# Performance work log

Hardware: AMD Instinct MI355X
Metric: run time of the kernel (lower is better)

The kernel has to match this reference:

```python
import jax, jax.numpy as jnp
import numpy as np

H = 768; B = 8; T = 1024; V = 50257
S = 256      # token_distribution_samples
K = 64       # token_topk
POOL = 1024  # max(S*4, K) token pool
TEMP = 0.1; LIM = 0.25; MW = 0.1


def _ln(x, g, b):
    m = x.mean(-1, keepdims=True)
    v = ((x - m) ** 2).mean(-1, keepdims=True)
    return (x - m) / jnp.sqrt(v + 1e-5) * g + b


def _head(x, g, b, w1, b1, w2, b2):
    # LayerNorm -> Linear -> GELU(exact) -> (Dropout=identity in eval) -> Linear
    h = _ln(x, g, b) @ w1 + b1
    h = jax.nn.gelu(h, approximate=False)
    return h @ w2 + b2


def _l2norm(x):
    return x / jnp.maximum(jnp.linalg.norm(x, axis=-1, keepdims=True), 1e-12)


def setup_inputs() -> dict:
    key = jax.random.key(0)
    ks = jax.random.split(key, 16)
    init = lambda k, shp: jax.random.normal(k, shp, jnp.float32) * 0.02
    f32 = jnp.float32
    return {
        "latent": jax.random.normal(ks[0], (B, T, H), f32),
        "token_embedding_matrix": jax.random.normal(ks[1], (V, H), f32),
        # scale head
        "scale_ln_g": jnp.ones((H,), f32), "scale_ln_b": jnp.zeros((H,), f32),
        "scale_w1": init(ks[2], (H, H)), "scale_b1": jnp.zeros((H,), f32),
        "scale_w2": init(ks[3], (H, H)), "scale_b2": jnp.zeros((H,), f32),
        # bias head
        "bias_ln_g": jnp.ones((H,), f32), "bias_ln_b": jnp.zeros((H,), f32),
        "bias_w1": init(ks[4], (H, H)), "bias_b1": jnp.zeros((H,), f32),
        "bias_w2": init(ks[5], (H, H)), "bias_b2": jnp.zeros((H,), f32),
        # contrastive head (projection_dim == H)
        "con_ln_g": jnp.ones((H,), f32), "con_ln_b": jnp.zeros((H,), f32),
        "con_w1": init(ks[6], (H, H)), "con_b1": jnp.zeros((H,), f32),
        "con_w2": init(ks[7], (H, H)), "con_b2": jnp.zeros((H,), f32),
        # deterministic augmentation noise (randn_like * 0.01)
        "noise_a": jax.random.normal(ks[8], (B * T, H), f32) * 0.01,
        "noise_b": jax.random.normal(ks[9], (B * T, H), f32) * 0.01,
        # deterministic row-sampling (torch.randperm analogues)
        "samp_idx": jax.random.permutation(ks[10], B * T)[:S].astype(jnp.int32),
        "tok_idx": jax.random.permutation(ks[11], V)[:POOL].astype(jnp.int32),
    }


def reference(latent, token_embedding_matrix,
              scale_ln_g, scale_ln_b, scale_w1, scale_b1, scale_w2, scale_b2,
              bias_ln_g, bias_ln_b, bias_w1, bias_b1, bias_w2, bias_b2,
              con_ln_g, con_ln_b, con_w1, con_b1, con_w2, con_b2,
              noise_a, noise_b, samp_idx, tok_idx):
    # compensate: u = s(z)*z + b(z)
    scale = 1.0 + LIM * jnp.tanh(_head(latent, scale_ln_g, scale_ln_b, scale_w1, scale_b1, scale_w2, scale_b2))
    bias = LIM * jnp.tanh(_head(latent, bias_ln_g, bias_ln_b, bias_w1, bias_b1, bias_w2, bias_b2))
    aligned = scale * latent + bias

    flat = aligned.reshape(-1, H)  # [N, H], N = B*T
    # contrastive loss
    va = _l2norm(_head(flat + noise_a, con_ln_g, con_ln_b, con_w1, con_b1, con_w2, con_b2))
    vb = _l2norm(_head(flat + noise_b, con_ln_g, con_ln_b, con_w1, con_b1, con_w2, con_b2))
    logits = va @ vb.T / TEMP  # [N, N]
    loss_ab = -jnp.mean(jnp.diagonal(jax.nn.log_softmax(logits, axis=-1)))
    loss_ba = -jnp.mean(jnp.diagonal(jax.nn.log_softmax(logits.T, axis=-1)))
    con_loss = 0.5 * (loss_ab + loss_ba)

    # token distribution loss
    af = flat[samp_idx]                     # [S, H]
    te = token_embedding_matrix[tok_idx]    # [POOL, H]
    tl = _l2norm(af) @ _l2norm(te).T / TEMP  # [S, POOL]
    top_vals, top_idx = jax.lax.top_k(tl, K)
    top_emb = te[top_idx]                   # [S, K, H] gather
    w = jax.nn.softmax(top_vals, axis=-1)[..., None]
    proto = (w * top_emb).sum(axis=1)       # [S, H]
    proto_loss = jnp.mean((af - proto) ** 2)
    moment_loss = jnp.mean((af.mean(0) - te.mean(0)) ** 2) \
        + jnp.mean((af.std(0) - te.std(0)) ** 2)
    token_dist_loss = proto_loss + MW * moment_loss

    comp_reg_loss = jnp.mean((scale - 1.0) ** 2) + jnp.mean(bias ** 2)
    return (aligned, con_loss, token_dist_loss, comp_reg_loss, scale, bias)
```

## Files before the change

### kernel.cpp

```cpp
#include <hip/hip_runtime.h>
#include <hip/hip_bf16.h>

typedef __hip_bfloat16 bf16;
typedef __attribute__((ext_vector_type(4))) float f32x4;
typedef __attribute__((ext_vector_type(8))) short bf16x8v;

static constexpr int   HD    = 768;
static constexpr int   NRr   = 8192;
static constexpr int   SSAMP = 256;
static constexpr int   KTOP  = 64;
static constexpr int   NPOOL = 1024;
static constexpr float TINV  = 10.0f;

__device__ __forceinline__ float bf2f(bf16 h){ return __bfloat162float(h); }
__device__ __forceinline__ bf16  f2bf(float f){ return __float2bfloat16(f); }

__device__ __forceinline__ float gelu_exact(float x){
  return 0.5f * x * (1.0f + erff(x * 0.70710678118654752f));
}

__device__ __forceinline__ float block_sum(float v, float* buf){
  const int lane = threadIdx.x & 63, w = threadIdx.x >> 6;
  const int nw = (int)blockDim.x >> 6;
  #pragma unroll
  for(int o = 32; o; o >>= 1) v += __shfl_down(v, o);
  __syncthreads();
  if(lane == 0) buf[w] = v;
  __syncthreads();
  float t = 0.f;
  for(int i = 0; i < nw; i++) t += buf[i];
  return t;
}

__device__ __forceinline__ void block_sum2(float& a, float& b, float* buf){
  const int lane = threadIdx.x & 63, w = threadIdx.x >> 6;
  #pragma unroll
  for(int o = 32; o; o >>= 1){ a += __shfl_down(a, o); b += __shfl_down(b, o); }
  __syncthreads();
  if(lane == 0){ buf[w] = a; buf[4 + w] = b; }
  __syncthreads();
  float ta = 0.f, tb = 0.f;
  #pragma unroll
  for(int i = 0; i < 4; i++){ ta += buf[i]; tb += buf[4 + i]; }
  a = ta; b = tb;
}

__device__ __forceinline__ void gload_lds16(const bf16* g, bf16* lds_uniform){
  __builtin_amdgcn_global_load_lds(
      (const __attribute__((address_space(1))) unsigned int*)(const void*)g,
      (__attribute__((address_space(3))) unsigned int*)(void*)lds_uniform,
      16, 0, 0);
}

struct TsA { const float* w[6]; const float* gg[6]; bf16* o[6]; };
__global__ __launch_bounds__(256)
void tscale6(TsA a){
  __shared__ float t[32][33];
  const int z = blockIdx.z;
  const float* Win = a.w[z];
  const float* g   = a.gg[z];
  bf16* Wt         = a.o[z];
  const int tx = threadIdx.x, ty = threadIdx.y;
  const int bx = blockIdx.x * 32, by = blockIdx.y * 32;
  #pragma unroll
  for(int j = 0; j < 4; j++)
    t[ty + j*8][tx] = Win[(size_t)(by + ty + j*8) * HD + bx + tx];
  __syncthreads();
  const float gv = g ? g[by + tx] : 1.0f;
  #pragma unroll
  for(int j = 0; j < 4; j++)
    Wt[(size_t)(bx + ty + j*8) * HD + by + tx] = f2bf(gv * t[tx][ty + j*8]);
}

struct FbA { const float* bln[3]; const float* w1[3]; const float* b1[3]; float* o[3]; };
__global__ __launch_bounds__(256)
void foldbias3(FbA a){
  __shared__ float red[4][64];
  const int h = blockIdx.y;
  const int lane = threadIdx.x & 63, w = threadIdx.x >> 6;
  const int n = blockIdx.x * 64 + lane;
  const float* bl = a.bln[h];
  const float* w1 = a.w1[h];
  float t = 0.f;
  for(int k = w * 192; k < w * 192 + 192; k++)
    t += bl[k] * w1[(size_t)k * HD + n];
  red[w][lane] = t;
  __syncthreads();
  if(w == 0)
    a.o[h][n] = a.b1[h][n] + red[0][lane] + red[1][lane] + red[2][lane] + red[3][lane];
}

__global__ __launch_bounds__(256)
void lnxh_kernel(const float* __restrict__ x, bf16* __restrict__ o){
  __shared__ float buf[4];
  const int row = blockIdx.x, tid = threadIdx.x;
  const size_t base = (size_t)row * HD;
  float v[3];
  #pragma unroll
  for(int j = 0; j < 3; j++) v[j] = x[base + tid + j*256];
  float s = v[0] + v[1] + v[2];
  s = block_sum(s, buf);
  const float m = s * (1.0f / HD);
  float q = 0.f;
  #pragma unroll
  for(int j = 0; j < 3; j++){ const float d = v[j] - m; q += d*d; }
  q = block_sum(q, buf);
  const float inv = rsqrtf(q * (1.0f / HD) + 1e-5f);
  #pragma unroll
  for(int j = 0; j < 3; j++)
    o[base + tid + j*256] = f2bf((v[j] - m) * inv);
}

__global__ __launch_bounds__(256)
void fuse_al_ln(const float* __restrict__ latent, const float* __restrict__ sc,
                const float* __restrict__ bi, const float* __restrict__ na,
                const float* __restrict__ nb, float* __restrict__ out_aligned,
                bf16* __restrict__ X){
  __shared__ float buf[8];
  const int row = blockIdx.x, tid = threadIdx.x;
  const size_t base = (size_t)row * HD;
  float ua[3], ub[3];
  #pragma unroll
  for(int j = 0; j < 3; j++){
    const int i = tid + j*256;
    const float a = sc[base + i] * latent[base + i] + bi[base + i];
    out_aligned[base + i] = a;
    ua[j] = a + na[base + i];
    ub[j] = a + nb[base + i];
  }
  float sa = ua[0] + ua[1] + ua[2];
  float sb = ub[0] + ub[1] + ub[2];
  block_sum2(sa, sb, buf);
  const float ma = sa * (1.0f / HD), mb = sb * (1.0f / HD);
  float qa = 0.f, qb = 0.f;
  #pragma unroll
  for(int j = 0; j < 3; j++){
    const float da = ua[j] - ma; qa += da*da;
    const float db = ub[j] - mb; qb += db*db;
  }
  block_sum2(qa, qb, buf);
  const float ia = rsqrtf(qa * (1.0f / HD) + 1e-5f);
  const float ib = rsqrtf(qb * (1.0f / HD) + 1e-5f);
  #pragma unroll
  for(int j = 0; j < 3; j++){
    const int i = tid + j*256;
    X[base + i] = f2bf((ua[j] - ma) * ia);
    X[(size_t)(row + NRr) * HD + i] = f2bf((ub[j] - mb) * ib);
  }
}

enum { EPI_GELU = 0, EPI_SB = 1, EPI_RAW = 3, EPI_LOGITS = 4, EPI_TL = 5 };

template<int EPI>
__global__ __launch_bounds__(256, 2)
void gemm_kernel(const bf16* __restrict__ A, const bf16* __restrict__ Bt,
                 const bf16* __restrict__ Bt2,
                 const int M, const int N, const int K,
                 const int lda, const int ldc,
                 const float* __restrict__ bias, const float* __restrict__ bias2,
                 bf16* __restrict__ outb, float* __restrict__ outf,
                 float* __restrict__ outf2,
                 float* __restrict__ aux, float* __restrict__ aux2){
  __shared__ __align__(16) bf16 As[128 * 64];
  __shared__ __align__(16) bf16 Bs[128 * 64];
  __shared__ float rbuf[512];

  const int tid  = threadIdx.x;
  const int wave = tid >> 6, lane = tid & 63;
  const int wm = wave >> 1, wn = wave & 1;
  const int r16 = lane & 15, kh = lane >> 4;
  const int bx = blockIdx.x, by = blockIdx.y;
  const int row0 = by * 128, col0 = bx * 128;

  float addv = 0.f;
  if constexpr(EPI == EPI_SB){
    if(blockIdx.z == 0){ addv = 1.0f; }
    else { A += 768; Bt = Bt2; bias = bias2; outf = outf2; }
  }

  f32x4 acc[4][4];
  #pragma unroll
  for(int i = 0; i < 4; i++)
    #pragma unroll
    for(int j = 0; j < 4; j++){ f32x4 z = {0.f,0.f,0.f,0.f}; acc[i][j] = z; }

  const bf16* gA[4]; const bf16* gB[4];
  bf16* lA[4]; bf16* lB[4];
  #pragma unroll
  for(int j = 0; j < 4; j++){
    const int c = tid + j*256;
    const int rr = c >> 3, p = c & 7;
    const int g = (p - (rr & 7)) & 7;
    gA[j] = A  + (size_t)(row0 + rr) * lda + g * 8;
    gB[j] = Bt + (size_t)(col0 + rr) * K   + g * 8;
    lA[j] = As + ((size_t)j*256 + wave*64) * 8;
    lB[j] = Bs + ((size_t)j*256 + wave*64) * 8;
  }
  const int sw = r16 & 7;

  for(int k0 = 0; k0 < K; k0 += 64){
    __syncthreads();
    #pragma unroll
    for(int j = 0; j < 4; j++){
      gload_lds16(gA[j] + k0, lA[j]);
      gload_lds16(gB[j] + k0, lB[j]);
    }
    __syncthreads();
    #pragma unroll
    for(int kk = 0; kk < 2; kk++){
      const int koff = ((kk*4 + kh + sw) & 7) * 8;
      bf16x8v av[4], bv[4];
      #pragma unroll
      for(int f = 0; f < 4; f++){
        av[f] = *(const bf16x8v*)(As + (wm*64 + f*16 + r16) * 64 + koff);
        bv[f] = *(const bf16x8v*)(Bs + (wn*64 + f*16 + r16) * 64 + koff);
      }
      #pragma unroll
      for(int i = 0; i < 4; i++)
        #pragma unroll
        for(int j = 0; j < 4; j++)
          acc[i][j] = __builtin_amdgcn_mfma_f32_16x16x32_bf16(av[i], bv[j], acc[i][j], 0, 0, 0);
    }
  }

  const int crow0 = row0 + wm * 64;
  const int ccol0 = col0 + wn * 64;

  if constexpr(EPI != EPI_LOGITS){
    float part = 0.f;
    #pragma unroll
    for(int i = 0; i < 4; i++){
      #pragma unroll
      for(int j = 0; j < 4; j++){
        const int col = ccol0 + j*16 + r16;
        const float bvv = bias ? bias[col] : 0.f;
        #pragma unroll
        for(int q = 0; q < 4; q++){
          const int row = crow0 + i*16 + kh*4 + q;
          const float v = acc[i][j][q] + bvv;
          const size_t off = (size_t)row * ldc + col;
          if constexpr(EPI == EPI_GELU){
            outb[off] = f2bf(gelu_exact(v));
          } else if constexpr(EPI == EPI_SB){
            const float t = 0.25f * tanhf(v);
            outf[off] = t + addv;
            part += t * t;
          } else if constexpr(EPI == EPI_TL){
            outf[off] = v * TINV;
          } else {
            outb[off] = f2bf(v);
          }
        }
      }
    }
    if constexpr(EPI == EPI_SB){
      const float tot2 = block_sum(part, rbuf);
      if(tid == 0)
        aux[(size_t)blockIdx.z * (gridDim.x * gridDim.y) + by * gridDim.x + bx] = tot2;
    }
  } else {
    float rs[16], cs[4];
    #pragma unroll
    for(int t = 0; t < 16; t++) rs[t] = 0.f;
    #pragma unroll
    for(int t = 0; t < 4; t++) cs[t] = 0.f;
    #pragma unroll
    for(int i = 0; i < 4; i++)
      #pragma unroll
      for(int j = 0; j < 4; j++)
        #pragma unroll
        for(int q = 0; q < 4; q++){
          const float ev = expf(acc[i][j][q] * TINV);
          rs[i*4 + q] += ev;
          cs[j]       += ev;
        }
    #pragma unroll
    for(int t = 0; t < 16; t++){
      float r = rs[t];
      r += __shfl_xor(r, 1); r += __shfl_xor(r, 2);
      r += __shfl_xor(r, 4); r += __shfl_xor(r, 8);
      rs[t] = r;
    }
    if(r16 == 0){
      #pragma unroll
      for(int i = 0; i < 4; i++)
        #pragma unroll
        for(int q = 0; q < 4; q++)
          rbuf[wn*128 + wm*64 + i*16 + kh*4 + q] = rs[i*4 + q];
    }
    #pragma unroll
    for(int j = 0; j < 4; j++){
      float c = cs[j];
      c += __shfl_xor(c, 16); c += __shfl_xor(c, 32);
      cs[j] = c;
    }
    if(kh == 0){
      #pragma unroll
      for(int j = 0; j < 4; j++)
        rbuf[256 + wm*128 + wn*64 + j*16 + r16] = cs[j];
    }
    __syncthreads();
    if(tid < 128){
      aux [(size_t)bx * M + row0 + tid] = rbuf[tid]       + rbuf[128 + tid];
      aux2[(size_t)by * M + col0 + tid] = rbuf[256 + tid] + rbuf[384 + tid];
    }
  }
}

__global__ __launch_bounds__(256)
void l2n_kernel(bf16* __restrict__ vio){
  __shared__ float buf[4];
  const int row = blockIdx.x, tid = threadIdx.x;
  const size_t base = (size_t)row * HD;
  float v[3];
  #pragma unroll
  for(int j = 0; j < 3; j++) v[j] = bf2f(vio[base + tid + j*256]);
  float q = v[0]*v[0] + v[1]*v[1] + v[2]*v[2];
  q = block_sum(q, buf);
  const float inv = 1.0f / fmaxf(sqrtf(q), 1e-12f);
  #pragma unroll
  for(int j = 0; j < 3; j++) vio[base + tid + j*256] = f2bf(v[j] * inv);
}

__global__ __launch_bounds__(256)
void rcdiag_kernel(const float* __restrict__ rp, const float* __restrict__ cp,
                   float* __restrict__ rs, float* __restrict__ cs, const int nb,
                   const bf16* __restrict__ va, const bf16* __restrict__ vb,
                   float* __restrict__ diag){
  if(blockIdx.x < 32){
    const int i = blockIdx.x * 256 + threadIdx.x;
    float r = 0.f, c = 0.f;
    for(int b = 0; b < nb; b++){
      r += rp[(size_t)b * NRr + i];
      c += cp[(size_t)b * NRr + i];
    }
    rs[i] = r; cs[i] = c;
  } else {
    const int lane = threadIdx.x & 63;
    const int row = (blockIdx.x - 32) * 4 + (threadIdx.x >> 6);
    const size_t base = (size_t)row * HD;
    float d = 0.f;
    #pragma unroll
    for(int j = 0; j < 12; j++){
      const int i = lane + j*64;
      d += bf2f(va[base + i]) * bf2f(vb[base + i]);
    }
    #pragma unroll
    for(int o = 32; o; o >>= 1) d += __shfl_down(d, o);
    if(lane == 0) diag[row] = d * TINV;
  }
}

__global__ __launch_bounds__(256)
void gather_kernel(const float* __restrict__ aligned, const int* __restrict__ samp,
                   float* __restrict__ afraw, bf16* __restrict__ afn,
                   const float* __restrict__ emb, const int* __restrict__ tok,
                   float* __restrict__ teg, bf16* __restrict__ ten){
  __shared__ float buf[4];
  const int tid = threadIdx.x;
  if(blockIdx.x < SSAMP){
    const int s = blockIdx.x;
    const size_t src = (size_t)samp[s] * HD, dst = (size_t)s * HD;
    float v[3];
    #pragma unroll
    for(int j = 0; j < 3; j++){
      const int i = tid + j*256;
      v[j] = aligned[src + i];
      afraw[dst + i] = v[j];
    }
    float q = v[0]*v[0] + v[1]*v[1] + v[2]*v[2];
    q = block_sum(q, buf);
    const float inv = 1.0f / fmaxf(sqrtf(q), 1e-12f);
    #pragma unroll
    for(int j = 0; j < 3; j++) afn[dst + tid + j*256] = f2bf(v[j] * inv);
  } else {
    const int p = blockIdx.x - SSAMP;
    const size_t src = (size_t)tok[p] * HD, dst = (size_t)p * HD;
    float v[3];
    #pragma unroll
    for(int j = 0; j < 3; j++){
      const int i = tid + j*256;
      v[j] = emb[src + i];
      teg[dst + i] = v[j];
    }
    float q = v[0]*v[0] + v[1]*v[1] + v[2]*v[2];
    q = block_sum(q, buf);
    const float inv = 1.0f / fmaxf(sqrtf(q), 1e-12f);
    #pragma unroll
    for(int j = 0; j < 3; j++) ten[dst + tid + j*256] = f2bf(v[j] * inv);
  }
}

__global__ __launch_bounds__(256)
void topk_kernel(const float* __restrict__ tl, const float* __restrict__ teg,
                 const float* __restrict__ afraw, float* __restrict__ protopart){
  __shared__ float sv[NPOOL];
  __shared__ float topv[KTOP];
  __shared__ int   topi[KTOP];
  __shared__ float wts[KTOP];
  __shared__ float rv[4];
  __shared__ int   ri[4];
  __shared__ float buf[4];
  __shared__ float sinv;
  const int s = blockIdx.x, tid = threadIdx.x;
  const int lane = tid & 63, w = tid >> 6;
  #pragma unroll
  for(int j = 0; j < 4; j++) sv[tid + j*256] = tl[(size_t)s * NPOOL + tid + j*256];
  __syncthreads();
  for(int k = 0; k < KTOP; k++){
    float bvv = -1e30f; int bi = 0x7fffffff;
    #pragma unroll
    for(int j = 0; j < 4; j++){
      const int i = tid + j*256;
      const float x = sv[i];
      if(x > bvv || (x == bvv && i < bi)){ bvv = x; bi = i; }
    }
    #pragma unroll
    for(int o = 1; o < 64; o <<= 1){
      const float ov = __shfl_xor(bvv, o);
      const int   oi = __shfl_xor(bi, o);
      if(ov > bvv || (ov == bvv && oi < bi)){ bvv = ov; bi = oi; }
    }
    if(lane == 0){ rv[w] = bvv; ri[w] = bi; }
    __syncthreads();
    if(tid == 0){
      for(int w2 = 1; w2 < 4; w2++)
        if(rv[w2] > bvv || (rv[w2] == bvv && ri[w2] < bi)){ bvv = rv[w2]; bi = ri[w2]; }
      if(bi < 0 || bi >= NPOOL) bi = 0;
      topv[k] = bvv; topi[k] = bi; sv[bi] = -1e30f;
    }
    __syncthreads();
  }
  if(tid < KTOP) wts[tid] = expf(topv[tid] - topv[0]);
  __syncthreads();
  if(tid == 0){
    float t = 0.f;
    for(int k = 0; k < KTOP; k++) t += wts[k];
    sinv = 1.0f / t;
  }
  __syncthreads();
  float part = 0.f;
  #pragma unroll
  for(int j = 0; j < 3; j++){
    const int h = tid + j*256;
    float ph = 0.f;
    for(int k = 0; k < KTOP; k++) ph += wts[k] * teg[(size_t)topi[k] * HD + h];
    ph *= sinv;
    const float d = afraw[(size_t)s * HD + h] - ph;
    part += d * d;
  }
  part = block_sum(part, buf);
  if(tid == 0) protopart[s] = part;
}

__global__ __launch_bounds__(768)
void mom1_kernel(const float* __restrict__ afraw, const float* __restrict__ teg,
                 float* __restrict__ partial){
  const int b = blockIdx.x, h = threadIdx.x;
  float sa = 0.f, sa2 = 0.f, st = 0.f, st2 = 0.f;
  for(int r = b * 40; r < b * 40 + 40; r++){
    if(r < SSAMP){
      const float v = afraw[(size_t)r * HD + h];
      sa += v; sa2 += v * v;
    } else {
      const float v = teg[(size_t)(r - SSAMP) * HD + h];
      st += v; st2 += v * v;
    }
  }
  partial[(size_t)(b*4 + 0) * HD + h] = sa;
  partial[(size_t)(b*4 + 1) * HD + h] = sa2;
  partial[(size_t)(b*4 + 2) * HD + h] = st;
  partial[(size_t)(b*4 + 3) * HD + h] = st2;
}

__global__ __launch_bounds__(768)
void mom2_kernel(const float* __restrict__ partial, float* __restrict__ mom){
  __shared__ float buf[12];
  const int h = threadIdx.x;
  float sa = 0.f, sa2 = 0.f, st = 0.f, st2 = 0.f;
  for(int b = 0; b < 32; b++){
    sa  += partial[(size_t)(b*4 + 0) * HD + h];
    sa2 += partial[(size_t)(b*4 + 1) * HD + h];
    st  += partial[(size_t)(b*4 + 2) * HD + h];
    st2 += partial[(size_t)(b*4 + 3) * HD + h];
  }
  const float ma  = sa * (1.0f / SSAMP);
  const float sda = sqrtf(fmaxf(sa2 * (1.0f / SSAMP) - ma * ma, 0.f));
  const float mt  = st * (1.0f / NPOOL);
  const float sdt = sqrtf(fmaxf(st2 * (1.0f / NPOOL) - mt * mt, 0.f));
  const float dmu = ma - mt, dsd = sda - sdt;
  const float t1 = block_sum(dmu * dmu, buf);
  const float t2 = block_sum(dsd * dsd, buf);
  if(h == 0){ mom[0] = t1; mom[1] = t2; }
}

__global__ __launch_bounds__(1024)
void final_kernel(const float* __restrict__ rs, const float* __restrict__ cs,
                  const float* __restrict__ diag,
                  const float* __restrict__ aux, const int naux,
                  const float* __restrict__ protopart, const float* __restrict__ mom,
                  float* __restrict__ outsc){
  __shared__ float buf[16];
  const int tid = threadIdx.x;
  float s1 = 0.f, s2 = 0.f;
  for(int r = tid; r < NRr; r += 1024){
    const float dg = diag[r];
    s1 += logf(rs[r]) - dg;
    s2 += logf(cs[r]) - dg;
  }
  float c1 = 0.f;
  for(int j = tid; j < naux; j += 1024) c1 += aux[j];
  float pp = 0.f;
  for(int j = tid; j < SSAMP; j += 1024) pp += protopart[j];
  s1 = block_sum(s1, buf);
  s2 = block_sum(s2, buf);
  c1 = block_sum(c1, buf);
  pp = block_sum(pp, buf);
  if(tid == 0){
    const float con  = 0.5f * (s1 + s2) / (float)NRr;
    const float creg = c1 / 6291456.0f;
    const float tdl  = pp / (float)(SSAMP * HD) + 0.1f * ((mom[0] + mom[1]) / (float)HD);
    outsc[0] = con;
    outsc[1] = tdl;
    outsc[2] = creg;
  }
}

extern "C" void kernel_launch(void* const* d_in, const int* in_sizes, int n_in,
                              void* d_out, int out_size, void* d_ws, size_t ws_size,
                              hipStream_t stream){
  (void)in_sizes; (void)n_in; (void)out_size; (void)ws_size;
  const float* latent = (const float*)d_in[0];
  const float* tokemb = (const float*)d_in[1];
  const float* s_g  = (const float*)d_in[2];  const float* s_bln = (const float*)d_in[3];
  const float* s_w1 = (const float*)d_in[4];  const float* s_b1  = (const float*)d_in[5];
  const float* s_w2 = (const float*)d_in[6];  const float* s_b2  = (const float*)d_in[7];
  const float* b_g  = (const float*)d_in[8];  const float* b_bln = (const float*)d_in[9];
  const float* b_w1 = (const float*)d_in[10]; const float* b_b1  = (const float*)d_in[11];
  const float* b_w2 = (const float*)d_in[12]; const float* b_b2  = (const float*)d_in[13];
  const float* c_g  = (const float*)d_in[14]; const float* c_bln = (const float*)d_in[15];
  const float* c_w1 = (const float*)d_in[16]; const float* c_b1  = (const float*)d_in[17];
  const float* c_w2 = (const float*)d_in[18]; const float* c_b2  = (const float*)d_in[19];
  const float* noise_a = (const float*)d_in[20];
  const float* noise_b = (const float*)d_in[21];
  const int*  samp = (const int*)d_in[22];
  const int*  tok  = (const int*)d_in[23];

  float* out = (float*)d_out;
  float* out_aligned = out;
  float* out_scalars = out + (size_t)NRr * HD;
  float* out_scale   = out + (size_t)NRr * HD + 3;
  float* out_bias    = out_scale + (size_t)NRr * HD;

  char* wp = (char*)d_ws;
  auto alloc = [&](size_t bytes) -> char* {
    char* p = wp; wp += (bytes + 255) & ~(size_t)255; return p;
  };
  bf16* wt_comb1 = (bf16*)alloc((size_t)2*HD*HD*2);
  bf16* wt_c1    = (bf16*)alloc((size_t)HD*HD*2);
  bf16* wt_s2    = (bf16*)alloc((size_t)HD*HD*2);
  bf16* wt_b2    = (bf16*)alloc((size_t)HD*HD*2);
  bf16* wt_c2    = (bf16*)alloc((size_t)HD*HD*2);
  float* bcomb1  = (float*)alloc(2*HD*4);
  float* bc1     = (float*)alloc(HD*4);
  bf16* A1 = (bf16*)alloc((size_t)2*NRr*HD*2);
  bf16* A2 = (bf16*)alloc((size_t)2*NRr*HD*2);
  float* rowpart = (float*)alloc((size_t)64*NRr*4);
  float* colpart = (float*)alloc((size_t)64*NRr*4);
  float* rowsum  = (float*)alloc((size_t)NRr*4);
  float* colsum  = (float*)alloc((size_t)NRr*4);
  float* diag    = (float*)alloc((size_t)NRr*4);
  float* aux     = (float*)alloc(768*4);
  float* afraw   = (float*)alloc((size_t)SSAMP*HD*4);
  float* teg     = (float*)alloc((size_t)NPOOL*HD*4);
  float* tlb     = (float*)alloc((size_t)SSAMP*NPOOL*4);
  float* protopart = (float*)alloc(SSAMP*4);
  float* mom     = (float*)alloc(2*4);
  float* mompart = rowpart;
  bf16*  ten     = (bf16*)colpart;
  bf16*  afn     = (bf16*)(colpart + ((size_t)NPOOL*HD*2)/4);

  TsA ts;
  ts.w[0]=s_w1; ts.gg[0]=s_g;     ts.o[0]=wt_comb1;
  ts.w[1]=b_w1; ts.gg[1]=b_g;     ts.o[1]=wt_comb1 + (size_t)HD*HD;
  ts.w[2]=c_w1; ts.gg[2]=c_g;     ts.o[2]=wt_c1;
  ts.w[3]=s_w2; ts.gg[3]=nullptr; ts.o[3]=wt_s2;
  ts.w[4]=b_w2; ts.gg[4]=nullptr; ts.o[4]=wt_b2;
  ts.w[5]=c_w2; ts.gg[5]=nullptr; ts.o[5]=wt_c2;
  tscale6<<<dim3(24,24,6), dim3(32,8), 0, stream>>>(ts);
  FbA fb;
  fb.bln[0]=s_bln; fb.w1[0]=s_w1; fb.b1[0]=s_b1; fb.o[0]=bcomb1;
  fb.bln[1]=b_bln; fb.w1[1]=b_w1; fb.b1[1]=b_b1; fb.o[1]=bcomb1 + HD;
  fb.bln[2]=c_bln; fb.w1[2]=c_w1; fb.b1[2]=c_b1; fb.o[2]=bc1;
  foldbias3<<<dim3(12,3), 256, 0, stream>>>(fb);

  lnxh_kernel<<<NRr, 256, 0, stream>>>(latent, A2);
  gemm_kernel<EPI_GELU><<<dim3(12,64), 256, 0, stream>>>(
      A2, wt_comb1, nullptr, NRr, 2*HD, HD, HD, 2*HD, bcomb1, nullptr,
      A1, nullptr, nullptr, nullptr, nullptr);
  gemm_kernel<EPI_SB><<<dim3(6,64,2), 256, 0, stream>>>(
      A1, wt_s2, wt_b2, NRr, HD, HD, 2*HD, HD, s_b2, b_b2,
      nullptr, out_scale, out_bias, aux, nullptr);

  fuse_al_ln<<<NRr, 256, 0, stream>>>(latent, out_scale, out_bias,
                                      noise_a, noise_b, out_aligned, A1);

  gemm_kernel<EPI_GELU><<<dim3(6,128), 256, 0, stream>>>(
      A1, wt_c1, nullptr, 2*NRr, HD, HD, HD, HD, bc1, nullptr,
      A2, nullptr, nullptr, nullptr, nullptr);
  gemm_kernel<EPI_RAW><<<dim3(6,128), 256, 0, stream>>>(
      A2, wt_c2, nullptr, 2*NRr, HD, HD, HD, HD, c_b2, nullptr,
      A1, nullptr, nullptr, nullptr, nullptr);
  l2n_kernel<<<2*NRr, 256, 0, stream>>>(A1);
  bf16* va = A1;
  bf16* vb = A1 + (size_t)NRr * HD;

  gemm_kernel<EPI_LOGITS><<<dim3(64,64), 256, 0, stream>>>(
      va, vb, nullptr, NRr, NRr, HD, HD, 0, nullptr, nullptr,
      nullptr, nullptr, nullptr, rowpart, colpart);
  rcdiag_kernel<<<32 + NRr/4, 256, 0, stream>>>(rowpart, colpart, rowsum, colsum, 64,
                                                va, vb, diag);

  gather_kernel<<<SSAMP + NPOOL, 256, 0, stream>>>(out_aligned, samp, afraw, afn,
                                                   tokemb, tok, teg, ten);
  gemm_kernel<EPI_TL><<<dim3(8,2), 256, 0, stream>>>(
      afn, ten, nullptr, SSAMP, NPOOL, HD, HD, NPOOL, nullptr, nullptr,
      nullptr, tlb, nullptr, nullptr, nullptr);
  topk_kernel<<<SSAMP, 256, 0, stream>>>(tlb, teg, afraw, protopart);
  mom1_kernel<<<32, 768, 0, stream>>>(afraw, teg, mompart);
  mom2_kernel<<<1, 768, 0, stream>>>(mompart, mom);

  final_kernel<<<1, 1024, 0, stream>>>(rowsum, colsum, diag, aux, 768,
                                       protopart, mom, out_scalars);
}
```

Baseline: 511.7 us.

## Fuse L2-norm with diagonal, token-logit GEMM into top-k, moments into final

L2-normalisation of the va and vb rows is merged with the diagonal logit computation in one kernel, and the row/column partial-sum reduction gets its own smaller kernel. The small token-logit GEMM is removed: each top-k block now computes its 1024 scaled dot products directly from the bf16 normalised embeddings, with the sample row held in shared memory. The second moment-reduction kernel is folded into the final scalar kernel. This cuts several launches and intermediate buffers. The cost is that every top-k block re-reads the full pool embedding matrix with per-thread strided vector loads and scalar FMAs instead of matrix-core instructions.

```diff
diff --git a/kernel.cpp b/kernel.cpp
--- a/kernel.cpp
+++ b/kernel.cpp
@@ -149,7 +149,7 @@
   }
 }
 
-enum { EPI_GELU = 0, EPI_SB = 1, EPI_RAW = 3, EPI_LOGITS = 4, EPI_TL = 5 };
+enum { EPI_GELU = 0, EPI_SB = 1, EPI_RAW = 3, EPI_LOGITS = 4 };
 
 template<int EPI>
 __global__ __launch_bounds__(256, 2)
@@ -245,8 +245,6 @@
             const float t = 0.25f * tanhf(v);
             outf[off] = t + addv;
             part += t * t;
-          } else if constexpr(EPI == EPI_TL){
-            outf[off] = v * TINV;
           } else {
             outb[off] = f2bf(v);
           }
@@ -308,47 +306,45 @@
 }
 
 __global__ __launch_bounds__(256)
-void l2n_kernel(bf16* __restrict__ vio){
-  __shared__ float buf[4];
+void l2ndiag_kernel(bf16* __restrict__ vab, float* __restrict__ diag){
+  __shared__ float buf[8];
   const int row = blockIdx.x, tid = threadIdx.x;
-  const size_t base = (size_t)row * HD;
-  float v[3];
-  #pragma unroll
-  for(int j = 0; j < 3; j++) v[j] = bf2f(vio[base + tid + j*256]);
-  float q = v[0]*v[0] + v[1]*v[1] + v[2]*v[2];
-  q = block_sum(q, buf);
-  const float inv = 1.0f / fmaxf(sqrtf(q), 1e-12f);
-  #pragma unroll
-  for(int j = 0; j < 3; j++) vio[base + tid + j*256] = f2bf(v[j] * inv);
-}
-
-__global__ __launch_bounds__(256)
-void rcdiag_kernel(const float* __restrict__ rp, const float* __restrict__ cp,
-                   float* __restrict__ rs, float* __restrict__ cs, const int nb,
-                   const bf16* __restrict__ va, const bf16* __restrict__ vb,
-                   float* __restrict__ diag){
-  if(blockIdx.x < 32){
-    const int i = blockIdx.x * 256 + threadIdx.x;
-    float r = 0.f, c = 0.f;
-    for(int b = 0; b < nb; b++){
-      r += rp[(size_t)b * NRr + i];
-      c += cp[(size_t)b * NRr + i];
-    }
-    rs[i] = r; cs[i] = c;
-  } else {
-    const int lane = threadIdx.x & 63;
-    const int row = (blockIdx.x - 32) * 4 + (threadIdx.x >> 6);
-    const size_t base = (size_t)row * HD;
-    float d = 0.f;
-    #pragma unroll
-    for(int j = 0; j < 12; j++){
-      const int i = lane + j*64;
-      d += bf2f(va[base + i]) * bf2f(vb[base + i]);
-    }
-    #pragma unroll
-    for(int o = 32; o; o >>= 1) d += __shfl_down(d, o);
-    if(lane == 0) diag[row] = d * TINV;
-  }
+  const size_t basea = (size_t)row * HD;
+  const size_t baseb = basea + (size_t)NRr * HD;
+  float a[3], b[3];
+  #pragma unroll
+  for(int j = 0; j < 3; j++){
+    a[j] = bf2f(vab[basea + tid + j*256]);
+    b[j] = bf2f(vab[baseb + tid + j*256]);
+  }
+  float qa = a[0]*a[0] + a[1]*a[1] + a[2]*a[2];
+  float qb = b[0]*b[0] + b[1]*b[1] + b[2]*b[2];
+  block_sum2(qa, qb, buf);
+  const float ia = 1.0f / fmaxf(sqrtf(qa), 1e-12f);
+  const float ib = 1.0f / fmaxf(sqrtf(qb), 1e-12f);
+  float d = 0.f;
+  #pragma unroll
+  for(int j = 0; j < 3; j++){
+    const bf16 oa = f2bf(a[j] * ia);
+    const bf16 ob = f2bf(b[j] * ib);
+    vab[basea + tid + j*256] = oa;
+    vab[baseb + tid + j*256] = ob;
+    d += bf2f(oa) * bf2f(ob);
+  }
+  d = block_sum(d, buf);
+  if(tid == 0) diag[row] = d * TINV;
+}
+
+__global__ __launch_bounds__(256)
+void rcsum_kernel(const float* __restrict__ rp, const float* __restrict__ cp,
+                  float* __restrict__ rs, float* __restrict__ cs, const int nb){
+  const int i = blockIdx.x * 256 + threadIdx.x;
+  float r = 0.f, c = 0.f;
+  for(int b = 0; b < nb; b++){
+    r += rp[(size_t)b * NRr + i];
+    c += cp[(size_t)b * NRr + i];
+  }
+  rs[i] = r; cs[i] = c;
 }
 
 __global__ __launch_bounds__(256)
@@ -392,8 +388,10 @@
 }
 
 __global__ __launch_bounds__(256)
-void topk_kernel(const float* __restrict__ tl, const float* __restrict__ teg,
-                 const float* __restrict__ afraw, float* __restrict__ protopart){
+void topk_kernel(const bf16* __restrict__ afn, const bf16* __restrict__ ten,
+                 const float* __restrict__ teg, const float* __restrict__ afraw,
+                 float* __restrict__ protopart){
+  __shared__ float saf[HD];
   __shared__ float sv[NPOOL];
   __shared__ float topv[KTOP];
   __shared__ int   topi[KTOP];
@@ -405,7 +403,21 @@
   const int s = blockIdx.x, tid = threadIdx.x;
   const int lane = tid & 63, w = tid >> 6;
   #pragma unroll
-  for(int j = 0; j < 4; j++) sv[tid + j*256] = tl[(size_t)s * NPOOL + tid + j*256];
+  for(int j = 0; j < 3; j++) saf[tid + j*256] = bf2f(afn[(size_t)s * HD + tid + j*256]);
+  __syncthreads();
+  #pragma unroll
+  for(int cb = 0; cb < 4; cb++){
+    const int c = tid + cb * 256;
+    const bf16* tr = ten + (size_t)c * HD;
+    float d = 0.f;
+    for(int k = 0; k < HD; k += 8){
+      int4 rawv = *(const int4*)(tr + k);
+      const bf16* e = (const bf16*)&rawv;
+      #pragma unroll
+      for(int u = 0; u < 8; u++) d += bf2f(e[u]) * saf[k + u];
+    }
+    sv[c] = d * TINV;
+  }
   __syncthreads();
   for(int k = 0; k < KTOP; k++){
     float bvv = -1e30f; int bi = 0x7fffffff;
@@ -473,32 +485,12 @@
   partial[(size_t)(b*4 + 3) * HD + h] = st2;
 }
 
-__global__ __launch_bounds__(768)
-void mom2_kernel(const float* __restrict__ partial, float* __restrict__ mom){
-  __shared__ float buf[12];
-  const int h = threadIdx.x;
-  float sa = 0.f, sa2 = 0.f, st = 0.f, st2 = 0.f;
-  for(int b = 0; b < 32; b++){
-    sa  += partial[(size_t)(b*4 + 0) * HD + h];
-    sa2 += partial[(size_t)(b*4 + 1) * HD + h];
-    st  += partial[(size_t)(b*4 + 2) * HD + h];
-    st2 += partial[(size_t)(b*4 + 3) * HD + h];
-  }
-  const float ma  = sa * (1.0f / SSAMP);
-  const float sda = sqrtf(fmaxf(sa2 * (1.0f / SSAMP) - ma * ma, 0.f));
-  const float mt  = st * (1.0f / NPOOL);
-  const float sdt = sqrtf(fmaxf(st2 * (1.0f / NPOOL) - mt * mt, 0.f));
-  const float dmu = ma - mt, dsd = sda - sdt;
-  const float t1 = block_sum(dmu * dmu, buf);
-  const float t2 = block_sum(dsd * dsd, buf);
-  if(h == 0){ mom[0] = t1; mom[1] = t2; }
-}
-
 __global__ __launch_bounds__(1024)
 void final_kernel(const float* __restrict__ rs, const float* __restrict__ cs,
                   const float* __restrict__ diag,
                   const float* __restrict__ aux, const int naux,
-                  const float* __restrict__ protopart, const float* __restrict__ mom,
+                  const float* __restrict__ protopart,
+                  const float* __restrict__ mompart,
                   float* __restrict__ outsc){
   __shared__ float buf[16];
   const int tid = threadIdx.x;
@@ -512,14 +504,32 @@
   for(int j = tid; j < naux; j += 1024) c1 += aux[j];
   float pp = 0.f;
   for(int j = tid; j < SSAMP; j += 1024) pp += protopart[j];
+  float t1p = 0.f, t2p = 0.f;
+  if(tid < HD){
+    float sa = 0.f, sa2 = 0.f, st = 0.f, st2 = 0.f;
+    for(int b = 0; b < 32; b++){
+      sa  += mompart[(size_t)(b*4 + 0) * HD + tid];
+      sa2 += mompart[(size_t)(b*4 + 1) * HD + tid];
+      st  += mompart[(size_t)(b*4 + 2) * HD + tid];
+      st2 += mompart[(size_t)(b*4 + 3) * HD + tid];
+    }
+    const float ma  = sa * (1.0f / SSAMP);
+    const float sda = sqrtf(fmaxf(sa2 * (1.0f / SSAMP) - ma * ma, 0.f));
+    const float mt  = st * (1.0f / NPOOL);
+    const float sdt = sqrtf(fmaxf(st2 * (1.0f / NPOOL) - mt * mt, 0.f));
+    const float dmu = ma - mt, dsd = sda - sdt;
+    t1p = dmu * dmu; t2p = dsd * dsd;
+  }
   s1 = block_sum(s1, buf);
   s2 = block_sum(s2, buf);
   c1 = block_sum(c1, buf);
   pp = block_sum(pp, buf);
+  const float t1 = block_sum(t1p, buf);
+  const float t2 = block_sum(t2p, buf);
   if(tid == 0){
     const float con  = 0.5f * (s1 + s2) / (float)NRr;
     const float creg = c1 / 6291456.0f;
-    const float tdl  = pp / (float)(SSAMP * HD) + 0.1f * ((mom[0] + mom[1]) / (float)HD);
+    const float tdl  = pp / (float)(SSAMP * HD) + 0.1f * ((t1 + t2) / (float)HD);
     outsc[0] = con;
     outsc[1] = tdl;
     outsc[2] = creg;
@@ -573,9 +583,7 @@
   float* aux     = (float*)alloc(768*4);
   float* afraw   = (float*)alloc((size_t)SSAMP*HD*4);
   float* teg     = (float*)alloc((size_t)NPOOL*HD*4);
-  float* tlb     = (float*)alloc((size_t)SSAMP*NPOOL*4);
   float* protopart = (float*)alloc(SSAMP*4);
-  float* mom     = (float*)alloc(2*4);
   float* mompart = rowpart;
   bf16*  ten     = (bf16*)colpart;
   bf16*  afn     = (bf16*)(colpart + ((size_t)NPOOL*HD*2)/4);
@@ -611,25 +619,20 @@
   gemm_kernel<EPI_RAW><<<dim3(6,128), 256, 0, stream>>>(
       A2, wt_c2, nullptr, 2*NRr, HD, HD, HD, HD, c_b2, nullptr,
       A1, nullptr, nullptr, nullptr, nullptr);
-  l2n_kernel<<<2*NRr, 256, 0, stream>>>(A1);
+  l2ndiag_kernel<<<NRr, 256, 0, stream>>>(A1, diag);
   bf16* va = A1;
   bf16* vb = A1 + (size_t)NRr * HD;
 
   gemm_kernel<EPI_LOGITS><<<dim3(64,64), 256, 0, stream>>>(
       va, vb, nullptr, NRr, NRr, HD, HD, 0, nullptr, nullptr,
       nullptr, nullptr, nullptr, rowpart, colpart);
-  rcdiag_kernel<<<32 + NRr/4, 256, 0, stream>>>(rowpart, colpart, rowsum, colsum, 64,
-                                                va, vb, diag);
+  rcsum_kernel<<<NRr / 256, 256, 0, stream>>>(rowpart, colpart, rowsum, colsum, 64);
 
   gather_kernel<<<SSAMP + NPOOL, 256, 0, stream>>>(out_aligned, samp, afraw, afn,
                                                    tokemb, tok, teg, ten);
-  gemm_kernel<EPI_TL><<<dim3(8,2), 256, 0, stream>>>(
-      afn, ten, nullptr, SSAMP, NPOOL, HD, HD, NPOOL, nullptr, nullptr,
-      nullptr, tlb, nullptr, nullptr, nullptr);
-  topk_kernel<<<SSAMP, 256, 0, stream>>>(tlb, teg, afraw, protopart);
+  topk_kernel<<<SSAMP, 256, 0, stream>>>(afn, ten, teg, afraw, protopart);
   mom1_kernel<<<32, 768, 0, stream>>>(afraw, teg, mompart);
-  mom2_kernel<<<1, 768, 0, stream>>>(mompart, mom);
 
   final_kernel<<<1, 1024, 0, stream>>>(rowsum, colsum, diag, aux, 768,
-                                       protopart, mom, out_scalars);
-}
+                                       protopart, mompart, out_scalars);
+}
```

Result: no change. 518.5 us (+1.3%).
